# Optimization experiments

Measured on AMD Instinct MI355X. Metric: run time of the kernel, lower is better.

The kernel has to match this reference:

```python
import jax, jax.numpy as jnp
import numpy as np

B, C_IN, H, W = 4, 256, 200, 176
A = 6            # anchors per location (3 sizes x 2 rotations)
NUM_CLS = 4      # 3 classes + background
K = 100
N_ANCH = A * H * W


def setup_inputs() -> dict:
    key = jax.random.key(0)
    k1, k2, k3, k4, k5, k6 = jax.random.split(key, 6)
    x = jax.random.normal(k1, (B, C_IN, H, W), dtype=jnp.float32)
    scale = 1.0 / np.sqrt(C_IN)
    cls_w = jax.random.normal(k2, (NUM_CLS * A, C_IN), dtype=jnp.float32) * scale
    cls_b = jnp.zeros((NUM_CLS * A,), dtype=jnp.float32)
    reg_w = jax.random.normal(k3, (7 * A, C_IN), dtype=jnp.float32) * scale * 0.1
    reg_b = jnp.zeros((7 * A,), dtype=jnp.float32)
    # anchors: [N,7] = (x, y, z, dx, dy, dz, ry) with strictly positive sizes
    xyz = jax.random.uniform(k4, (N_ANCH, 3), minval=-35.0, maxval=35.0)
    sizes = jax.random.uniform(k5, (N_ANCH, 3), minval=1.0, maxval=4.0)
    rot = jax.random.uniform(k6, (N_ANCH, 1), minval=-np.pi, maxval=np.pi)
    anchors = jnp.concatenate([xyz, sizes, rot], axis=-1).astype(jnp.float32)
    return {"x": x, "cls_w": cls_w, "cls_b": cls_b,
            "reg_w": reg_w, "reg_b": reg_b, "anchors": anchors}


def _decode(deltas, anchors):
    # SECOND-style residual box decoder.  deltas, anchors: [B, N, 7]
    xa, ya, za, dxa, dya, dza, ra = jnp.split(anchors, 7, axis=-1)
    xt, yt, zt, dxt, dyt, dzt, rt = jnp.split(deltas, 7, axis=-1)
    diag = jnp.sqrt(dxa * dxa + dya * dya)
    xg = xt * diag + xa
    yg = yt * diag + ya
    zg = zt * dza + za
    dxg = jnp.exp(dxt) * dxa
    dyg = jnp.exp(dyt) * dya
    dzg = jnp.exp(dzt) * dza
    rg = rt + ra
    return jnp.concatenate([xg, yg, zg, dxg, dyg, dzg, rg], axis=-1)


def reference(x, cls_w, cls_b, reg_w, reg_b, anchors):
    # 1x1 conv heads: [B,C_in,H,W] -> [B,C_out,H,W]
    cls_pred = jnp.einsum('bchw,oc->bohw', x, cls_w) + cls_b[None, :, None, None]
    reg_pred = jnp.einsum('bchw,oc->bohw', x, reg_w) + reg_b[None, :, None, None]
    # permute(0,2,3,1).reshape(B, num_anchors, -1)
    cls_pred = jnp.transpose(cls_pred, (0, 2, 3, 1)).reshape(B, N_ANCH, NUM_CLS)
    reg_pred = jnp.transpose(reg_pred, (0, 2, 3, 1)).reshape(B, N_ANCH, 7)
    batch_anchors = jnp.broadcast_to(anchors[None], (B, N_ANCH, 7))
    pred_bboxes = _decode(reg_pred, batch_anchors)
    pred_scores = jax.nn.softmax(cls_pred, axis=-1)
    # per-frame top-k over max foreground score (classes 1:)
    max_scores = jnp.max(pred_scores[..., 1:], axis=-1)      # [B, N]
    _, topk_inds = jax.lax.top_k(max_scores, K)              # [B, K]
    topk_bboxes = jnp.take_along_axis(pred_bboxes, topk_inds[..., None], axis=1)
    topk_scores = jnp.take_along_axis(pred_scores, topk_inds[..., None], axis=1)
    return (topk_scores, topk_bboxes)
```

## Files before the change

### kernel.cpp

```cpp
#include <hip/hip_runtime.h>

#define BB 4
#define CIN 256
#define HW 35200
#define AA 6
#define NANCH (AA * HW)
#define TOPK 100
#define NBIN 4096
#define BINBASE 28416
#define CAP 4096
#define SMAX 4096
#define TILES 550
#define ZEROWORDS (BB * NBIN + 16)

__device__ __forceinline__ unsigned sbin(unsigned bits) {
  int v = (int)(bits >> 15) - BINBASE;
  v = v < 0 ? 0 : v;
  v = v > (NBIN - 1) ? (NBIN - 1) : v;
  return (unsigned)v;
}

__device__ __forceinline__ float sc4(float4 l) {
  float m = fmaxf(fmaxf(l.x, l.y), fmaxf(l.z, l.w));
  float e0 = expf(l.x - m), e1 = expf(l.y - m);
  float e2 = expf(l.z - m), e3 = expf(l.w - m);
  return fmaxf(fmaxf(e1, e2), e3) / (e0 + e1 + e2 + e3);
}

#define FMA4(A, W, S)                                      \
  A.x = fmaf(S, W.x, A.x); A.y = fmaf(S, W.y, A.y);        \
  A.z = fmaf(S, W.z, A.z); A.w = fmaf(S, W.w, A.w);

__global__ __launch_bounds__(256) void k0_init(
    const float* __restrict__ cls_w, float* __restrict__ wt,
    unsigned int* __restrict__ zr) {
  int t = blockIdx.x * 256 + threadIdx.x;
  int stride = gridDim.x * 256;
  for (int i = t; i < ZEROWORDS; i += stride) zr[i] = 0u;
  for (int i = t; i < 24 * CIN; i += stride)
    wt[(i % CIN) * 24 + (i / CIN)] = cls_w[i];
}

__global__ __launch_bounds__(256, 3) void k1_scores(
    const float* __restrict__ x, const float* __restrict__ wt,
    const float* __restrict__ cls_b, unsigned int* __restrict__ hist,
    float* __restrict__ maxsc) {
  int bid = blockIdx.x;
  int b = bid / TILES, tile = bid % TILES;
  int tid = threadIdx.x;

  __shared__ unsigned lh[NBIN];
  __shared__ float sred[4][64][24];
  for (int i = tid; i < NBIN; i += 256) lh[i] = 0;

  int l = tid & 63;
  int s = __builtin_amdgcn_readfirstlane(tid >> 6);
  int hw = tile * 64 + l;
  const float* xb = x + (size_t)b * CIN * HW + hw;
  int c0 = s * 64;

  float4 a0 = make_float4(0.f, 0.f, 0.f, 0.f), a1 = a0, a2 = a0;
  float4 a3 = a0, a4 = a0, a5 = a0;

#pragma unroll 1
  for (int cc = 0; cc < 64; cc += 8) {
    float xv[8];
#pragma unroll
    for (int u = 0; u < 8; ++u)
      xv[u] = xb[(size_t)(c0 + cc + u) * HW];
#pragma unroll
    for (int u = 0; u < 8; ++u) {
      const float4* wr = (const float4*)(wt + (c0 + cc + u) * 24);
      float4 w0 = wr[0], w1 = wr[1], w2 = wr[2];
      float4 w3 = wr[3], w4 = wr[4], w5 = wr[5];
      float v = xv[u];
      FMA4(a0, w0, v) FMA4(a1, w1, v) FMA4(a2, w2, v)
      FMA4(a3, w3, v) FMA4(a4, w4, v) FMA4(a5, w5, v)
    }
  }

  float4* sp = (float4*)&sred[s][l][0];
  sp[0] = a0; sp[1] = a1; sp[2] = a2; sp[3] = a3; sp[4] = a4; sp[5] = a5;
  __syncthreads();

  const float4* bias4 = (const float4*)cls_b;
  for (int task = tid; task < 384; task += 256) {
    int a = task % 6, h = task / 6;
    float4 v0 = ((const float4*)&sred[0][h][0])[a];
    float4 v1 = ((const float4*)&sred[1][h][0])[a];
    float4 v2 = ((const float4*)&sred[2][h][0])[a];
    float4 v3 = ((const float4*)&sred[3][h][0])[a];
    float4 vb = bias4[a];
    float4 v;
    v.x = v0.x + v1.x + v2.x + v3.x + vb.x;
    v.y = v0.y + v1.y + v2.y + v3.y + vb.y;
    v.z = v0.z + v1.z + v2.z + v3.z + vb.z;
    v.w = v0.w + v1.w + v2.w + v3.w + vb.w;
    float sc = sc4(v);
    unsigned n = (unsigned)(tile * 64 + h) * 6u + (unsigned)a;
    maxsc[(size_t)b * NANCH + n] = sc;
    atomicAdd(&lh[sbin(__float_as_uint(sc))], 1u);
  }
  __syncthreads();
  unsigned* gh = hist + (size_t)b * NBIN;
  for (int i = tid; i < NBIN; i += 256) {
    unsigned c = lh[i];
    if (c) atomicAdd(&gh[i], c);
  }
}

__global__ __launch_bounds__(256) void k2_thresh(
    const unsigned int* __restrict__ hist, unsigned int* __restrict__ thresh) {
  int b = blockIdx.x, tid = threadIdx.x;
  const unsigned* h = hist + (size_t)b * NBIN;
  unsigned r[16];
  unsigned s = 0;
#pragma unroll
  for (int i = 0; i < 16; ++i) { r[i] = h[tid * 16 + i]; s += r[i]; }
  __shared__ unsigned seg[256];
  seg[tid] = s;
  __syncthreads();
  for (int d = 1; d < 256; d <<= 1) {
    unsigned add = (tid + d < 256) ? seg[tid + d] : 0u;
    __syncthreads();
    seg[tid] += add;
    __syncthreads();
  }
  unsigned above = (tid < 255) ? seg[tid + 1] : 0u;
  if (above < TOPK && above + s >= TOPK) {
    unsigned c = above, T = 0;
    for (int i = 15; i >= 0; --i) {
      c += r[i];
      if (c >= TOPK) { T = tid * 16u + (unsigned)i; break; }
    }
    thresh[b] = T;
  }
}

__global__ __launch_bounds__(256) void k3_compact(
    const float* __restrict__ maxsc, const unsigned int* __restrict__ thresh,
    unsigned int* __restrict__ cand_count, unsigned long long* __restrict__ cand) {
  unsigned p = blockIdx.x * 256u + threadIdx.x;
  unsigned b = p / NANCH, n = p % NANCH;
  unsigned bits = __float_as_uint(maxsc[p]);
  bool pred = sbin(bits) >= thresh[b];
  unsigned long long mask = __ballot(pred);
  if (mask) {
    int lane = threadIdx.x & 63;
    int leader = (int)__ffsll(mask) - 1;
    unsigned base = 0;
    if (lane == leader)
      base = atomicAdd(&cand_count[b], (unsigned)__popcll(mask));
    base = __shfl(base, leader, 64);
    if (pred) {
      unsigned pos = base + (unsigned)__popcll(mask & ((1ull << lane) - 1ull));
      if (pos < CAP)
        cand[(size_t)b * CAP + pos] =
            ((unsigned long long)bits << 32) | (unsigned)(~n);
    }
  }
}

__global__ __launch_bounds__(256) void k4_sort(
    const unsigned long long* __restrict__ cand,
    const unsigned int* __restrict__ cand_count, unsigned int* __restrict__ topk) {
  int b = blockIdx.x, tid = threadIdx.x;
  __shared__ unsigned long long sh[SMAX];
  unsigned cnt = cand_count[b];
  if (cnt > CAP) cnt = CAP;
  unsigned S = 128;
  while (S < cnt) S <<= 1;
  for (unsigned t = tid; t < S; t += 256)
    sh[t] = (t < cnt) ? cand[(size_t)b * CAP + t] : 0ULL;
  __syncthreads();
  for (unsigned kk = 2; kk <= S; kk <<= 1) {
    for (unsigned jj = kk >> 1; jj > 0; jj >>= 1) {
      for (unsigned t = tid; t < S; t += 256) {
        unsigned ixj = t ^ jj;
        if (ixj > t) {
          unsigned long long a = sh[t], c = sh[ixj];
          bool sw = ((t & kk) == 0) ? (a < c) : (a > c);
          if (sw) { sh[t] = c; sh[ixj] = a; }
        }
      }
      __syncthreads();
    }
  }
  if (tid < TOPK)
    topk[b * TOPK + tid] = ~(unsigned)(sh[tid] & 0xFFFFFFFFULL);
}

__global__ __launch_bounds__(256) void k5_out(
    const float* __restrict__ x, const float* __restrict__ cls_w,
    const float* __restrict__ cls_b, const float* __restrict__ reg_w,
    const float* __restrict__ reg_b, const float* __restrict__ anchors,
    const unsigned int* __restrict__ topk, float* __restrict__ out) {
  int bk = blockIdx.x;
  int b = bk / TOPK, k = bk % TOPK;
  unsigned n = topk[b * TOPK + k];
  int a = (int)(n % AA);
  unsigned hw = n / AA;
  int tid = threadIdx.x;

  float xv = x[(size_t)b * CIN * HW + (size_t)tid * HW + hw];
  float part[11];
#pragma unroll
  for (int j = 0; j < 4; ++j) part[j] = xv * cls_w[(a * 4 + j) * CIN + tid];
#pragma unroll
  for (int j = 0; j < 7; ++j) part[4 + j] = xv * reg_w[(a * 7 + j) * CIN + tid];

#pragma unroll
  for (int j = 0; j < 11; ++j) {
    float v = part[j];
    for (int off = 32; off > 0; off >>= 1) v += __shfl_down(v, off, 64);
    part[j] = v;
  }
  __shared__ float red[4][11];
  int wave = tid >> 6, lane = tid & 63;
  if (lane == 0) {
#pragma unroll
    for (int j = 0; j < 11; ++j) red[wave][j] = part[j];
  }
  __syncthreads();
  if (tid == 0) {
    float tot[11];
#pragma unroll
    for (int j = 0; j < 11; ++j)
      tot[j] = red[0][j] + red[1][j] + red[2][j] + red[3][j];
    float l0 = tot[0] + cls_b[a * 4 + 0];
    float l1 = tot[1] + cls_b[a * 4 + 1];
    float l2 = tot[2] + cls_b[a * 4 + 2];
    float l3 = tot[3] + cls_b[a * 4 + 3];
    float m = fmaxf(fmaxf(l0, l1), fmaxf(l2, l3));
    float e0 = expf(l0 - m), e1 = expf(l1 - m);
    float e2 = expf(l2 - m), e3 = expf(l3 - m);
    float inv = 1.0f / (e0 + e1 + e2 + e3);
    float* os = out + ((size_t)b * TOPK + k) * 4;
    os[0] = e0 * inv; os[1] = e1 * inv; os[2] = e2 * inv; os[3] = e3 * inv;
    const float* an = anchors + (size_t)n * 7;
    float xa = an[0], ya = an[1], za = an[2];
    float dxa = an[3], dya = an[4], dza = an[5], ra = an[6];
    float xt = tot[4] + reg_b[a * 7 + 0];
    float yt = tot[5] + reg_b[a * 7 + 1];
    float zt = tot[6] + reg_b[a * 7 + 2];
    float dxt = tot[7] + reg_b[a * 7 + 3];
    float dyt = tot[8] + reg_b[a * 7 + 4];
    float dzt = tot[9] + reg_b[a * 7 + 5];
    float rt = tot[10] + reg_b[a * 7 + 6];
    float diag = sqrtf(dxa * dxa + dya * dya);
    float* ob = out + (size_t)BB * TOPK * 4 + ((size_t)b * TOPK + k) * 7;
    ob[0] = xt * diag + xa;
    ob[1] = yt * diag + ya;
    ob[2] = zt * dza + za;
    ob[3] = expf(dxt) * dxa;
    ob[4] = expf(dyt) * dya;
    ob[5] = expf(dzt) * dza;
    ob[6] = rt + ra;
  }
}

extern "C" void kernel_launch(void* const* d_in, const int* in_sizes, int n_in,
                              void* d_out, int out_size, void* d_ws, size_t ws_size,
                              hipStream_t stream) {
  const float* x       = (const float*)d_in[0];
  const float* cls_w   = (const float*)d_in[1];
  const float* cls_b   = (const float*)d_in[2];
  const float* reg_w   = (const float*)d_in[3];
  const float* reg_b   = (const float*)d_in[4];
  const float* anchors = (const float*)d_in[5];
  float* out = (float*)d_out;

  char* ws = (char*)d_ws;
  unsigned int* hist       = (unsigned int*)(ws);
  unsigned int* cand_count = (unsigned int*)(ws + 65536);
  unsigned int* thresh     = (unsigned int*)(ws + 65600);
  unsigned int* topk       = (unsigned int*)(ws + 65664);
  float* wt                = (float*)(ws + 67712);
  unsigned long long* cand = (unsigned long long*)(ws + 92288);
  float* maxsc             = (float*)(ws + 223360);

  k0_init<<<80, 256, 0, stream>>>(cls_w, wt, hist);
  k1_scores<<<BB * TILES, 256, 0, stream>>>(x, wt, cls_b, hist, maxsc);
  k2_thresh<<<BB, 256, 0, stream>>>(hist, thresh);
  k3_compact<<<(BB * NANCH) / 256, 256, 0, stream>>>(maxsc, thresh, cand_count, cand);
  k4_sort<<<BB, 256, 0, stream>>>(cand, cand_count, topk);
  k5_out<<<BB * TOPK, 256, 0, stream>>>(x, cls_w, cls_b, reg_w, reg_b, anchors,
                                        topk, out);
}
```

Before: 268.6 us.

## Restructure score kernel: 2 pixels per thread, LDS weights, 2-way channel split

The score kernel now has each thread handle two adjacent pixels using float2 loads, and splits channels across 2 groups instead of 4. This halves the cross-wave reduction and reuses each weight load across two pixels. The transposed classifier weights now live in shared memory, filled per block, instead of being staged through a global workspace by the init kernel. The grid drops from 550 to 138 tiles per batch and occupancy is lowered to 2 blocks per SM. The trade is extra LDS use, 24KB for weights per block, a per-block weight transpose, and fewer blocks, which may reduce latency hiding for the memory-bound x reads.

```diff
diff --git a/kernel.cpp b/kernel.cpp
--- a/kernel.cpp
+++ b/kernel.cpp
@@ -10,7 +10,7 @@
 #define BINBASE 28416
 #define CAP 4096
 #define SMAX 4096
-#define TILES 550
+#define TILES 138
 #define ZEROWORDS (BB * NBIN + 16)
 
 __device__ __forceinline__ unsigned sbin(unsigned bits) {
@@ -31,75 +31,88 @@
   A.x = fmaf(S, W.x, A.x); A.y = fmaf(S, W.y, A.y);        \
   A.z = fmaf(S, W.z, A.z); A.w = fmaf(S, W.w, A.w);
 
-__global__ __launch_bounds__(256) void k0_init(
-    const float* __restrict__ cls_w, float* __restrict__ wt,
-    unsigned int* __restrict__ zr) {
+__global__ __launch_bounds__(256) void k0_init(unsigned int* __restrict__ zr) {
   int t = blockIdx.x * 256 + threadIdx.x;
   int stride = gridDim.x * 256;
   for (int i = t; i < ZEROWORDS; i += stride) zr[i] = 0u;
-  for (int i = t; i < 24 * CIN; i += stride)
-    wt[(i % CIN) * 24 + (i / CIN)] = cls_w[i];
-}
-
-__global__ __launch_bounds__(256, 3) void k1_scores(
-    const float* __restrict__ x, const float* __restrict__ wt,
+}
+
+__global__ __launch_bounds__(256, 2) void k1_scores(
+    const float* __restrict__ x, const float* __restrict__ cls_w,
     const float* __restrict__ cls_b, unsigned int* __restrict__ hist,
     float* __restrict__ maxsc) {
   int bid = blockIdx.x;
   int b = bid / TILES, tile = bid % TILES;
   int tid = threadIdx.x;
 
+  __shared__ __align__(16) float swf[CIN * 24];
   __shared__ unsigned lh[NBIN];
-  __shared__ float sred[4][64][24];
+  __shared__ float4 sred[128][13];
+
+  for (int i = tid; i < CIN * 24; i += 256)
+    swf[(i % CIN) * 24 + (i / CIN)] = cls_w[i];
   for (int i = tid; i < NBIN; i += 256) lh[i] = 0;
-
-  int l = tid & 63;
-  int s = __builtin_amdgcn_readfirstlane(tid >> 6);
-  int hw = tile * 64 + l;
-  const float* xb = x + (size_t)b * CIN * HW + hw;
-  int c0 = s * 64;
-
-  float4 a0 = make_float4(0.f, 0.f, 0.f, 0.f), a1 = a0, a2 = a0;
-  float4 a3 = a0, a4 = a0, a5 = a0;
+  __syncthreads();
+
+  int l = tid & 127;
+  int s = tid >> 7;
+  int hw0 = tile * 256 + 2 * l;
+  bool act = hw0 < HW;
+  const float* xb = x + (size_t)b * CIN * HW + (act ? hw0 : 0);
+  int c0 = s * 128;
+
+  float4 acc[2][6];
+#pragma unroll
+  for (int h = 0; h < 2; ++h)
+#pragma unroll
+    for (int j = 0; j < 6; ++j) acc[h][j] = make_float4(0.f, 0.f, 0.f, 0.f);
 
 #pragma unroll 1
-  for (int cc = 0; cc < 64; cc += 8) {
-    float xv[8];
+  for (int cc = 0; cc < 128; cc += 8) {
+    float2 xv[8];
 #pragma unroll
     for (int u = 0; u < 8; ++u)
-      xv[u] = xb[(size_t)(c0 + cc + u) * HW];
+      xv[u] = *(const float2*)(xb + (size_t)(c0 + cc + u) * HW);
 #pragma unroll
     for (int u = 0; u < 8; ++u) {
-      const float4* wr = (const float4*)(wt + (c0 + cc + u) * 24);
+      const float4* wr = (const float4*)&swf[(c0 + cc + u) * 24];
       float4 w0 = wr[0], w1 = wr[1], w2 = wr[2];
       float4 w3 = wr[3], w4 = wr[4], w5 = wr[5];
-      float v = xv[u];
-      FMA4(a0, w0, v) FMA4(a1, w1, v) FMA4(a2, w2, v)
-      FMA4(a3, w3, v) FMA4(a4, w4, v) FMA4(a5, w5, v)
-    }
-  }
-
-  float4* sp = (float4*)&sred[s][l][0];
-  sp[0] = a0; sp[1] = a1; sp[2] = a2; sp[3] = a3; sp[4] = a4; sp[5] = a5;
-  __syncthreads();
-
-  const float4* bias4 = (const float4*)cls_b;
-  for (int task = tid; task < 384; task += 256) {
-    int a = task % 6, h = task / 6;
-    float4 v0 = ((const float4*)&sred[0][h][0])[a];
-    float4 v1 = ((const float4*)&sred[1][h][0])[a];
-    float4 v2 = ((const float4*)&sred[2][h][0])[a];
-    float4 v3 = ((const float4*)&sred[3][h][0])[a];
-    float4 vb = bias4[a];
-    float4 v;
-    v.x = v0.x + v1.x + v2.x + v3.x + vb.x;
-    v.y = v0.y + v1.y + v2.y + v3.y + vb.y;
-    v.z = v0.z + v1.z + v2.z + v3.z + vb.z;
-    v.w = v0.w + v1.w + v2.w + v3.w + vb.w;
-    float sc = sc4(v);
-    unsigned n = (unsigned)(tile * 64 + h) * 6u + (unsigned)a;
-    maxsc[(size_t)b * NANCH + n] = sc;
-    atomicAdd(&lh[sbin(__float_as_uint(sc))], 1u);
+      float x0 = xv[u].x, x1 = xv[u].y;
+      FMA4(acc[0][0], w0, x0) FMA4(acc[1][0], w0, x1)
+      FMA4(acc[0][1], w1, x0) FMA4(acc[1][1], w1, x1)
+      FMA4(acc[0][2], w2, x0) FMA4(acc[1][2], w2, x1)
+      FMA4(acc[0][3], w3, x0) FMA4(acc[1][3], w3, x1)
+      FMA4(acc[0][4], w4, x0) FMA4(acc[1][4], w4, x1)
+      FMA4(acc[0][5], w5, x0) FMA4(acc[1][5], w5, x1)
+    }
+  }
+
+  if (s == 1) {
+#pragma unroll
+    for (int j = 0; j < 6; ++j) {
+      sred[l][j] = acc[0][j];
+      sred[l][6 + j] = acc[1][j];
+    }
+  }
+  __syncthreads();
+  if (s == 0 && act) {
+    const float4* bias4 = (const float4*)cls_b;
+    float* mp = maxsc + (size_t)b * NANCH + (size_t)hw0 * 6u;
+#pragma unroll
+    for (int h = 0; h < 2; ++h) {
+#pragma unroll
+      for (int j = 0; j < 6; ++j) {
+        float4 v = acc[h][j];
+        float4 o = sred[l][h * 6 + j];
+        float4 bb = bias4[j];
+        v.x += o.x + bb.x; v.y += o.y + bb.y;
+        v.z += o.z + bb.z; v.w += o.w + bb.w;
+        float sc = sc4(v);
+        mp[h * 6 + j] = sc;
+        atomicAdd(&lh[sbin(__float_as_uint(sc))], 1u);
+      }
+    }
   }
   __syncthreads();
   unsigned* gh = hist + (size_t)b * NBIN;
@@ -275,12 +288,11 @@
   unsigned int* cand_count = (unsigned int*)(ws + 65536);
   unsigned int* thresh     = (unsigned int*)(ws + 65600);
   unsigned int* topk       = (unsigned int*)(ws + 65664);
-  float* wt                = (float*)(ws + 67712);
-  unsigned long long* cand = (unsigned long long*)(ws + 92288);
-  float* maxsc             = (float*)(ws + 223360);
-
-  k0_init<<<80, 256, 0, stream>>>(cls_w, wt, hist);
-  k1_scores<<<BB * TILES, 256, 0, stream>>>(x, wt, cls_b, hist, maxsc);
+  unsigned long long* cand = (unsigned long long*)(ws + 67712);
+  float* maxsc             = (float*)(ws + 198784);
+
+  k0_init<<<80, 256, 0, stream>>>(hist);
+  k1_scores<<<BB * TILES, 256, 0, stream>>>(x, cls_w, cls_b, hist, maxsc);
   k2_thresh<<<BB, 256, 0, stream>>>(hist, thresh);
   k3_compact<<<(BB * NANCH) / 256, 256, 0, stream>>>(maxsc, thresh, cand_count, cand);
   k4_sort<<<BB, 256, 0, stream>>>(cand, cand_count, topk);
```

Measured after the change: 273.3 us. About the same (+1.8%).
